# Optimization experiments

Measured on AMD Instinct MI355X. Metric: run time of the kernel, lower is better.

Reference implementation:

```python
import jax, jax.numpy as jnp
import numpy as np

B, T, D_MODEL = 2, 1024, 1024
HEAD_DIM = 128
NUM_HEADS = D_MODEL // HEAD_DIM          # 8
EXPAND_V = 1
HEAD_V = HEAD_DIM * EXPAND_V             # 128
KEY_DIM = NUM_HEADS * HEAD_DIM           # 1024
VALUE_DIM = NUM_HEADS * HEAD_V           # 1024
CONV_SIZE = 4
NUM_LEVELS = int(np.log2(T)) + 1         # 11 Fenwick levels
EPS = 1e-5
SCALE = HEAD_DIM ** -0.5


def setup_inputs() -> dict:
    ks = jax.random.split(jax.random.key(0), 20)
    w = lambda i, shp: 0.02 * jax.random.normal(ks[i], shp, jnp.float32)
    return {
        'x': jax.random.normal(ks[0], (B, T, D_MODEL), jnp.float32),
        'cos': jax.random.normal(ks[1], (T, HEAD_DIM), jnp.float32),
        'sin': jax.random.normal(ks[2], (T, HEAD_DIM), jnp.float32),
        'Wq': w(3, (D_MODEL, KEY_DIM)),
        'Wk': w(4, (D_MODEL, KEY_DIM)),
        'Wv': w(5, (D_MODEL, VALUE_DIM)),
        'Wb': w(6, (D_MODEL, NUM_HEADS)),
        'Wa': w(7, (D_MODEL, NUM_HEADS)),
        'Wl': w(8, (D_MODEL, NUM_HEADS * NUM_LEVELS)),
        'Wg': w(9, (D_MODEL, VALUE_DIM)),
        'Wo': w(10, (VALUE_DIM, D_MODEL)),
        'conv_q': 0.2 * jax.random.normal(ks[11], (KEY_DIM, CONV_SIZE), jnp.float32),
        'conv_k': 0.2 * jax.random.normal(ks[12], (KEY_DIM, CONV_SIZE), jnp.float32),
        'conv_v': 0.2 * jax.random.normal(ks[13], (VALUE_DIM, CONV_SIZE), jnp.float32),
        'A_log': jnp.log(jax.random.uniform(ks[14], (NUM_HEADS,), jnp.float32, 1.0, 16.0)),
        'dt_bias': jnp.log(jnp.expm1(jax.random.uniform(ks[15], (NUM_HEADS,), jnp.float32, 0.001, 0.1))),
        'norm_w': jnp.ones((HEAD_V,), jnp.float32),
    }


def _dwconv_silu(x, w):
    # causal depthwise conv1d (ShortConvolution, activation=silu). x:[B,T,C], w:[C,K]
    xp = jnp.pad(x, ((0, 0), (CONV_SIZE - 1, 0), (0, 0)))
    y = jax.lax.conv_general_dilated(xp, w.T[:, None, :], (1,), 'VALID',
                                     dimension_numbers=('NHC', 'HIO', 'NHC'),
                                     feature_group_count=w.shape[0])
    return jax.nn.silu(y)


def _l2norm(x):
    return x * jax.lax.rsqrt(jnp.sum(x * x, -1, keepdims=True) + 1e-6)


def _levels():
    # Fenwick-tree level of token s (0-indexed) in the prefix decomposition at time t:
    # level(t,s) = floor(log2((t+1) XOR s)) for s <= t.
    n = jnp.arange(1, T + 1, dtype=jnp.int32)[:, None]
    s = jnp.arange(T, dtype=jnp.int32)[None, :]
    xval = jnp.maximum(jnp.bitwise_xor(n, s), 1)
    lev = jnp.floor(jnp.log2(xval.astype(jnp.float32))).astype(jnp.int32)
    return jnp.clip(lev, 0, NUM_LEVELS - 1)  # [T,T]


def _forward(x, Wq, Wk, Wv, Wb, Wa, Wl, Wg, Wo, conv_q, conv_k, conv_v, A_log, dt_bias, norm_w):
    # projections + short conv + silu, split heads -> [B,H,T,d]
    q = _dwconv_silu(x @ Wq, conv_q).reshape(B, T, NUM_HEADS, HEAD_DIM).transpose(0, 2, 1, 3)
    k = _dwconv_silu(x @ Wk, conv_k).reshape(B, T, NUM_HEADS, HEAD_DIM).transpose(0, 2, 1, 3)
    v = _dwconv_silu(x @ Wv, conv_v).reshape(B, T, NUM_HEADS, HEAD_V).transpose(0, 2, 1, 3)
    q = _l2norm(q) * SCALE
    k = _l2norm(k)
    beta = jax.nn.sigmoid(x @ Wb).transpose(0, 2, 1)                      # [B,H,T]
    g = -jnp.exp(A_log) * jax.nn.softplus(x @ Wa + dt_bias)              # [B,T,H] log-decay per step
    gc = jnp.cumsum(g.transpose(0, 2, 1), axis=-1)                        # [B,H,T]
    lam = jax.nn.sigmoid(x @ Wl).reshape(B, T, NUM_HEADS, NUM_LEVELS).transpose(0, 2, 1, 3)  # [B,H,T,L]

    idx = jnp.arange(T)
    causal = idx[:, None] >= idx[None, :]
    strict = idx[:, None] > idx[None, :]
    # stable decay matrix D[t,s] = exp(gc_t - gc_s) <= 1 for s <= t
    logD = gc[..., :, None] - gc[..., None, :]
    Dm = jnp.exp(jnp.where(causal, logD, -jnp.inf))                       # [B,H,T,T]

    # WY / UT transform of the gated delta rule:
    #   u_t = beta_t * v_t - beta_t * sum_{s<t} (k_t . k_s) exp(gc_t-gc_s) u_s
    Akk = jnp.einsum('bhtd,bhsd->bhts', k, k) * Dm * strict
    u = jax.scipy.linalg.solve_triangular(beta[..., None] * Akk,
                                          beta[..., None] * v,
                                          lower=True, unit_diagonal=True)  # [B,H,T,dv]

    # log-linear (hierarchical) readout: o_t = sum_s lam_t[level(t,s)] * (q_t.k_s) D[t,s] * u_s
    P = jnp.einsum('bhtd,bhsd->bhts', q, k) * Dm
    M = jnp.take_along_axis(lam, _levels()[None, None], axis=3)           # [B,H,T,T]
    o = jnp.einsum('bhts,bhsd->bhtd', P * M, u).transpose(0, 2, 1, 3)      # [B,T,H,dv]

    # gated RMSNorm output gate, then output projection
    gate = (x @ Wg).reshape(B, T, NUM_HEADS, HEAD_V)
    o = o * jax.lax.rsqrt(jnp.mean(o * o, -1, keepdims=True) + EPS) * norm_w * jax.nn.silu(gate)
    return o.reshape(B, T, VALUE_DIM) @ Wo


def reference(x, cos, sin, Wq, Wk, Wv, Wb, Wa, Wl, Wg, Wo, conv_q, conv_k, conv_v, A_log, dt_bias, norm_w):
    # cos/sin are accepted (block signature) but unused, matching the source module.
    return _forward(x, Wq, Wk, Wv, Wb, Wa, Wl, Wg, Wo, conv_q, conv_k, conv_v, A_log, dt_bias, norm_w)
```

## Files before the change

### kernel.cpp

```cpp
#include <hip/hip_runtime.h>
#include <hip/hip_bf16.h>
#include <math.h>

#define SCALE_Q 0.08838834764831845f

typedef __bf16 bf16x8 __attribute__((ext_vector_type(8)));
typedef float f32x4 __attribute__((ext_vector_type(4)));

static __device__ __forceinline__ float sigm(float x){ return 1.f/(1.f+__expf(-x)); }
static __device__ __forceinline__ ushort f2b(float v){
  __hip_bfloat16 t = __float2bfloat16(v);
  return __builtin_bit_cast(ushort, t);
}

__global__ __launch_bounds__(256) void cast_x(const float* __restrict__ X,
    ushort* __restrict__ Y)
{
  int idx = blockIdx.x*256 + threadIdx.x;
  float4 v = *(const float4*)&X[(size_t)idx*4];
  ushort4 o; o.x=f2b(v.x); o.y=f2b(v.y); o.z=f2b(v.z); o.w=f2b(v.w);
  *(ushort4*)&Y[(size_t)idx*4] = o;
}

__global__ __launch_bounds__(256) void transcast(const float* __restrict__ W,
    ushort* __restrict__ Wt)
{
  __shared__ float tile[32][36];
  int n0 = blockIdx.x*32, k0 = blockIdx.y*32;
  int tid = threadIdx.x;
  int r = tid >> 3, c4 = (tid & 7) << 2;
  *(float4*)&tile[r][c4] = *(const float4*)&W[(size_t)(k0 + r)*1024 + n0 + c4];
  __syncthreads();
  ushort4 o;
  o.x = f2b(tile[c4+0][r]); o.y = f2b(tile[c4+1][r]);
  o.z = f2b(tile[c4+2][r]); o.w = f2b(tile[c4+3][r]);
  *(ushort4*)&Wt[(size_t)(n0 + r)*1024 + k0 + c4] = o;
}

__global__ __launch_bounds__(256) void copy_wsmall(const float* __restrict__ Wb,
    const float* __restrict__ Wa, const float* __restrict__ Wl, float* __restrict__ Wsm)
{
  int idx = blockIdx.x*256 + threadIdx.x;
  if (idx >= 1024*104) return;
  int k = idx / 104, c = idx % 104;
  float v = (c < 8) ? Wb[k*8+c] : (c < 16) ? Wa[k*8+(c-8)] : Wl[k*88+(c-16)];
  Wsm[idx] = v;
}

__global__ __launch_bounds__(256) void gemm_bf16(const ushort* __restrict__ A,
    const ushort* __restrict__ Bt, float* __restrict__ C0, float* __restrict__ C1,
    int M, int N, int K, int nsplit, int ld0, int ld1)
{
  __shared__ ushort As[128*32];
  __shared__ ushort Bs[128*32];
  int tid = threadIdx.x;
  int bm = blockIdx.y * 128, bn = blockIdx.x * 128;
  int wave = tid >> 6, lane = tid & 63;
  int wm = (wave >> 1) * 64, wn = (wave & 1) * 64;
  int l16 = lane & 15, kh = lane >> 4;
  f32x4 acc[4][4] = {};
  int rowA0 = tid >> 2, boA = (tid & 3) * 16;
  for (int k0 = 0; k0 < K; k0 += 32) {
    #pragma unroll
    for (int j = 0; j < 2; ++j) {
      int row = rowA0 + j*64;
      const char* gA = (const char*)A + (((size_t)(bm+row)*K + k0)*2 + boA);
      const char* gB = (const char*)Bt + (((size_t)(bn+row)*K + k0)*2 + boA);
      __builtin_amdgcn_global_load_lds((const __attribute__((address_space(1))) unsigned*)gA,
        (__attribute__((address_space(3))) unsigned*)((char*)As + row*64 + boA), 16, 0, 0);
      __builtin_amdgcn_global_load_lds((const __attribute__((address_space(1))) unsigned*)gB,
        (__attribute__((address_space(3))) unsigned*)((char*)Bs + row*64 + boA), 16, 0, 0);
    }
    __syncthreads();
    bf16x8 af[4], bfr[4];
    #pragma unroll
    for (int i = 0; i < 4; ++i)
      af[i] = *(bf16x8*)((char*)As + (wm + i*16 + l16)*64 + kh*16);
    #pragma unroll
    for (int j = 0; j < 4; ++j)
      bfr[j] = *(bf16x8*)((char*)Bs + (wn + j*16 + l16)*64 + kh*16);
    #pragma unroll
    for (int i = 0; i < 4; ++i)
      #pragma unroll
      for (int j = 0; j < 4; ++j)
        acc[i][j] = __builtin_amdgcn_mfma_f32_16x16x32_bf16(af[i], bfr[j], acc[i][j], 0, 0, 0);
    __syncthreads();
  }
  int rg = lane >> 4;
  #pragma unroll
  for (int i = 0; i < 4; ++i) {
    #pragma unroll
    for (int j = 0; j < 4; ++j) {
      int col = bn + wn + j*16 + l16;
      #pragma unroll
      for (int r = 0; r < 4; ++r) {
        int row = bm + wm + i*16 + rg*4 + r;
        float v = acc[i][j][r];
        if (col < nsplit) C0[(size_t)row*ld0 + col] = v;
        else              C1[(size_t)row*ld1 + (col - nsplit)] = v;
      }
    }
  }
}

__global__ __launch_bounds__(256) void skinny104(const float* __restrict__ X,
    const float* __restrict__ Wsm, float* __restrict__ part)
{
  __shared__ float XL[64][132];
  __shared__ float WsL[128][112];
  int tid = threadIdx.x;
  int m0 = blockIdx.x << 6;
  int k0 = blockIdx.y << 7;
  #pragma unroll
  for (int j = 0; j < 8; ++j) {
    int s = tid + j*256;
    int row = s >> 5, c4 = (s & 31) << 2;
    *(float4*)&XL[row][c4] = *(const float4*)&X[(size_t)(m0 + row)*1024 + k0 + c4];
  }
  {
    int k = tid >> 1, c = 104 + ((tid & 1) << 2);
    *(float4*)&WsL[k][c] = (float4){0.f,0.f,0.f,0.f};
  }
  {
    int k = tid >> 1, cb = (tid & 1) * 52;
    #pragma unroll
    for (int j = 0; j < 13; ++j) {
      *(float4*)&WsL[k][cb + j*4] = *(const float4*)&Wsm[(size_t)(k0 + k)*104 + cb + j*4];
    }
  }
  __syncthreads();
  int row = tid >> 2, cq = tid & 3;
  int cbase = cq * 28;
  f32x4 acc[7] = {};
  const float* xrow = &XL[row][0];
  #pragma unroll 4
  for (int k = 0; k < 128; ++k) {
    float xv = xrow[k];
    const f32x4* wr = (const f32x4*)&WsL[k][cbase];
    #pragma unroll
    for (int j = 0; j < 7; ++j) acc[j] += xv * wr[j];
  }
  float* pr = &part[((size_t)blockIdx.y*2048 + m0 + row)*104 + cbase];
  int nst = (cq == 3) ? 5 : 7;
  for (int j = 0; j < nst; ++j) *(f32x4*)&pr[j*4] = acc[j];
}

__global__ __launch_bounds__(256) void reduce8(const float* __restrict__ part,
    float* __restrict__ xs)
{
  int idx = blockIdx.x*256 + threadIdx.x;
  float s = 0.f;
  #pragma unroll
  for (int i = 0; i < 8; ++i) s += part[(size_t)i*212992 + idx];
  xs[idx] = s;
}

__global__ __launch_bounds__(256) void conv_silu(const float* __restrict__ X,
    const float* __restrict__ W, float* __restrict__ Yf, ushort* __restrict__ Yb,
    int mode, int ldx)
{
  int row = blockIdx.x;
  int b = row >> 10, t = row & 1023;
  int tid = threadIdx.x;
  int c0 = tid << 2;
  float w[4][4];
  #pragma unroll
  for (int c = 0; c < 4; ++c) {
    float4 wv = *(const float4*)&W[(c0 + c)*4];
    w[c][0]=wv.x; w[c][1]=wv.y; w[c][2]=wv.z; w[c][3]=wv.w;
  }
  float acc[4] = {0.f,0.f,0.f,0.f};
  #pragma unroll
  for (int j = 0; j < 4; ++j) {
    int tt = t - 3 + j;
    if (tt >= 0) {
      float4 xv = *(const float4*)&X[(size_t)(b*1024 + tt)*ldx + c0];
      acc[0] += w[0][j]*xv.x; acc[1] += w[1][j]*xv.y;
      acc[2] += w[2][j]*xv.z; acc[3] += w[3][j]*xv.w;
    }
  }
  #pragma unroll
  for (int c = 0; c < 4; ++c) acc[c] *= sigm(acc[c]);
  if (mode < 2) {
    float ss = acc[0]*acc[0]+acc[1]*acc[1]+acc[2]*acc[2]+acc[3]*acc[3];
    ss += __shfl_xor(ss, 1); ss += __shfl_xor(ss, 2); ss += __shfl_xor(ss, 4);
    ss += __shfl_xor(ss, 8); ss += __shfl_xor(ss, 16);
    float r = rsqrtf(ss + 1e-6f);
    if (mode == 0) r *= SCALE_Q;
    acc[0]*=r; acc[1]*=r; acc[2]*=r; acc[3]*=r;
  }
  size_t o = (size_t)(b*1024 + t)*1024 + c0;
  if (mode != 0) {
    float4 yv; yv.x=acc[0]; yv.y=acc[1]; yv.z=acc[2]; yv.w=acc[3];
    *(float4*)&Yf[o] = yv;
  }
  if (mode != 2) {
    ushort4 yb; yb.x=f2b(acc[0]); yb.y=f2b(acc[1]); yb.z=f2b(acc[2]); yb.w=f2b(acc[3]);
    *(ushort4*)&Yb[o] = yb;
  }
}

__global__ __launch_bounds__(256) void gc2(const float* __restrict__ xs,
    const float* __restrict__ A_log, const float* __restrict__ dt_bias,
    float* __restrict__ gc)
{
  int bh = blockIdx.x, b = bh >> 3, h = bh & 7;
  __shared__ float sc[256];
  int tid = threadIdx.x;
  float aexp = __expf(A_log[h]), db = dt_bias[h];
  int t0 = tid*4;
  float g[4], csum = 0.f;
  #pragma unroll
  for (int z = 0; z < 4; ++z) {
    float zv = xs[(size_t)(b*1024 + t0 + z)*104 + 8 + h] + db;
    float sp = (zv > 20.f) ? zv : log1pf(__expf(zv));
    csum += -aexp*sp;
    g[z] = csum;
  }
  sc[tid] = csum;
  __syncthreads();
  for (int ofs = 1; ofs < 256; ofs <<= 1) {
    float v = (tid >= ofs) ? sc[tid-ofs] : 0.f;
    __syncthreads();
    sc[tid] += v;
    __syncthreads();
  }
  float excl = sc[tid] - csum;
  #pragma unroll
  for (int z = 0; z < 4; ++z) gc[bh*1024 + t0 + z] = excl + g[z];
}

__global__ __launch_bounds__(256) void chunk_prep(const float* __restrict__ Kg,
    const float* __restrict__ Vg, const float* __restrict__ xs,
    const float* __restrict__ gcg, float* __restrict__ cw, ushort* __restrict__ cWk16,
    ushort* __restrict__ cKpT16, float* __restrict__ eD)
{
  int blk = blockIdx.x;
  int bh = blk >> 4, ck = blk & 15;
  int b = bh >> 3, h = bh & 7;
  int a = ck << 6;
  __shared__ float Kc[64][132];
  __shared__ float As[64][68];
  __shared__ float gcl[65];
  __shared__ float bl[64];
  __shared__ float egc[64];
  __shared__ float edt[64];
  int tid = threadIdx.x;
  for (int e = tid; e < 64*32; e += 256) {
    int t = e >> 5, c4 = (e & 31) << 2;
    *(float4*)&Kc[t][c4] = *(const float4*)&Kg[(size_t)(b*1024 + a + t)*1024 + h*128 + c4];
  }
  if (tid < 64) {
    gcl[tid] = gcg[bh*1024 + a + tid];
    bl[tid] = sigm(xs[(size_t)(b*1024 + a + tid)*104 + h]);
  }
  if (tid == 64) gcl[64] = (ck < 15) ? gcg[bh*1024 + a + 64] : 0.f;
  __syncthreads();
  if (tid < 64) {
    egc[tid] = __expf(gcl[tid] - gcl[0]);
    edt[tid] = (ck < 15) ? __expf(gcl[64] - gcl[tid]) : 0.f;
  }
  {
    int ti = tid >> 4, si = tid & 15;
    if (si <= ti) {
      float dot[4][4] = {};
      for (int kk = 0; kk < 128; kk += 4) {
        float4 kt[4], ks[4];
        #pragma unroll
        for (int z = 0; z < 4; ++z) kt[z] = *(float4*)&Kc[ti*4+z][kk];
        #pragma unroll
        for (int z = 0; z < 4; ++z) ks[z] = *(float4*)&Kc[si*4+z][kk];
        #pragma unroll
        for (int i = 0; i < 4; ++i)
          #pragma unroll
          for (int j = 0; j < 4; ++j)
            dot[i][j] += kt[i].x*ks[j].x + kt[i].y*ks[j].y + kt[i].z*ks[j].z + kt[i].w*ks[j].w;
      }
      #pragma unroll
      for (int i = 0; i < 4; ++i) {
        int t = ti*4 + i;
        #pragma unroll
        for (int j = 0; j < 4; ++j) {
          int s = si*4 + j;
          if (s < t) As[t][s] = bl[t]*dot[i][j]*__expf(gcl[t]-gcl[s]);
        }
      }
    }
  }
  __syncthreads();
  int c = tid;
  float u[64];
  if (c < 128) {
    #pragma unroll
    for (int t = 0; t < 64; ++t)
      u[t] = bl[t]*Vg[(size_t)(b*1024 + a + t)*1024 + h*128 + c];
  } else {
    int d = c - 128;
    #pragma unroll
    for (int t = 0; t < 64; ++t)
      u[t] = bl[t]*egc[t]*Kc[t][d];
  }
  #pragma unroll
  for (int t = 1; t < 64; ++t) {
    float acc = u[t];
    int s = 0;
    #pragma unroll
    for (; s + 4 <= t; s += 4) {
      float4 a4 = *(float4*)&As[t][s];
      acc -= a4.x*u[s] + a4.y*u[s+1] + a4.z*u[s+2] + a4.w*u[s+3];
    }
    #pragma unroll
    for (; s < t; ++s) acc -= As[t][s]*u[s];
    u[t] = acc;
  }
  size_t cbase = (size_t)blk*8192;
  if (c < 128) {
    #pragma unroll
    for (int t = 0; t < 64; ++t)
      cw[cbase + t*128 + c] = u[t];
  } else {
    int d = c - 128;
    #pragma unroll
    for (int t = 0; t < 64; ++t) {
      cWk16[cbase + t*128 + d] = f2b(-u[t]);
      cKpT16[cbase + d*64 + t] = f2b(Kc[t][d]*edt[t]);
    }
  }
  if (tid == 0) eD[blk] = (ck < 15) ? __expf(gcl[64]-gcl[0]) : 0.f;
}

__global__ __launch_bounds__(256) void chunk_scan6(const float* __restrict__ cw,
    const ushort* __restrict__ cWk16, const ushort* __restrict__ cKpT16,
    const float* __restrict__ eD, ushort* __restrict__ Ut)
{
  int blk = blockIdx.x;
  int slice = blk >> 4, bh = blk & 15;
  int e_base = slice << 3;
  __shared__ ushort Wks[2][8192];
  __shared__ ushort Kps[2][8192];
  __shared__ ushort StT[16*128];
  __shared__ ushort usT[16*64];
  __shared__ float  Stf[128*16];
  int tid = threadIdx.x;
  int wave = tid >> 6, lane = tid & 63;
  int l15 = lane & 15, kh = lane >> 4;
  for (int idx = tid; idx < 16*128; idx += 256) StT[idx] = 0;
  for (int idx = tid; idx < 16*64; idx += 256) usT[idx] = 0;
  for (int idx = tid; idx < 128*16; idx += 256) Stf[idx] = 0.f;

  int e = l15;
  int t0 = wave*16 + kh*4;
  int ci0 = bh << 4;
  f32x4 wcur = {0.f,0.f,0.f,0.f};
  if (e < 8) {
    #pragma unroll
    for (int r = 0; r < 4; ++r)
      wcur[r] = cw[(size_t)ci0*8192 + (t0+r)*128 + e_base + e];
  }
  {
    const char* wg = (const char*)(cWk16 + (size_t)ci0*8192);
    const char* kg = (const char*)(cKpT16 + (size_t)ci0*8192);
    #pragma unroll
    for (int j = 0; j < 4; ++j) {
      unsigned off = (j<<12) + (tid<<4);
      unsigned wrow = off >> 8, wslot = (off >> 4) & 15;
      unsigned wsrc = wrow*256 + ((wslot ^ (wrow & 15)) << 4);
      __builtin_amdgcn_global_load_lds((const __attribute__((address_space(1))) unsigned*)(wg + wsrc),
        (__attribute__((address_space(3))) unsigned*)((char*)&Wks[0][0] + off), 16, 0, 0);
      unsigned krow = off >> 7, kslot = (off >> 4) & 7;
      unsigned ksrc = krow*128 + ((kslot ^ (krow & 7)) << 4);
      __builtin_amdgcn_global_load_lds((const __attribute__((address_space(1))) unsigned*)(kg + ksrc),
        (__attribute__((address_space(3))) unsigned*)((char*)&Kps[0][0] + off), 16, 0, 0);
    }
  }
  __syncthreads();

  for (int i = 0; i < 16; ++i) {
    int ci = ci0 + i, a = i << 6, cur = i & 1;
    f32x4 wnext = {0.f,0.f,0.f,0.f};
    if (i < 15) {
      if (e < 8) {
        #pragma unroll
        for (int r = 0; r < 4; ++r)
          wnext[r] = cw[(size_t)(ci+1)*8192 + (t0+r)*128 + e_base + e];
      }
      const char* wg = (const char*)(cWk16 + (size_t)(ci+1)*8192);
      const char* kg = (const char*)(cKpT16 + (size_t)(ci+1)*8192);
      char* wl = (char*)&Wks[cur^1][0];
      char* kl = (char*)&Kps[cur^1][0];
      #pragma unroll
      for (int j = 0; j < 4; ++j) {
        unsigned off = (j<<12) + (tid<<4);
        unsigned wrow = off >> 8, wslot = (off >> 4) & 15;
        unsigned wsrc = wrow*256 + ((wslot ^ (wrow & 15)) << 4);
        __builtin_amdgcn_global_load_lds((const __attribute__((address_space(1))) unsigned*)(wg + wsrc),
          (__attribute__((address_space(3))) unsigned*)(wl + off), 16, 0, 0);
        unsigned krow = off >> 7, kslot = (off >> 4) & 7;
        unsigned ksrc = krow*128 + ((kslot ^ (krow & 7)) << 4);
        __builtin_amdgcn_global_load_lds((const __attribute__((address_space(1))) unsigned*)(kg + ksrc),
          (__attribute__((address_space(3))) unsigned*)(kl + off), 16, 0, 0);
      }
    }
    {
      f32x4 d = wcur;
      const char* wkb = (const char*)&Wks[cur][0];
      int arow = wave*16 + l15;
      #pragma unroll
      for (int ks = 0; ks < 4; ++ks) {
        bf16x8 afr = *(const bf16x8*)(wkb + arow*256 + (((ks*4 + kh) ^ l15) << 4));
        bf16x8 bfr = *(const bf16x8*)((const char*)StT + l15*256 + (((ks*4 + kh) ^ l15) << 4));
        d = __builtin_amdgcn_mfma_f32_16x16x32_bf16(afr, bfr, d, 0, 0, 0);
      }
      if (e < 8) {
        ushort4 uw;
        uw.x = f2b(d[0]); uw.y = f2b(d[1]); uw.z = f2b(d[2]); uw.w = f2b(d[3]);
        *(ushort4*)((char*)usT + e*128 + (((t0>>3) ^ (e&7)) << 4) + (t0&7)*2) = uw;
        *(ushort4*)&Ut[(size_t)(bh*128 + e_base + e)*1024 + a + t0] = uw;
      }
    }
    asm volatile("s_waitcnt lgkmcnt(0)" ::: "memory");
    __builtin_amdgcn_s_barrier();
    __builtin_amdgcn_sched_barrier(0);
    if (i < 15) {
      float ed = eD[ci];
      const char* kpb = (const char*)&Kps[cur][0];
      #pragma unroll
      for (int mt = 0; mt < 2; ++mt) {
        int krow = (wave*2 + mt)*16 + l15;
        int k0 = (wave*2 + mt)*16 + kh*4;
        f32x4 c;
        #pragma unroll
        for (int r = 0; r < 4; ++r) c[r] = ed * Stf[(k0+r)*16 + e];
        #pragma unroll
        for (int ts = 0; ts < 2; ++ts) {
          bf16x8 afr = *(const bf16x8*)(kpb + krow*128 + (((ts*4 + kh) ^ (krow&7)) << 4));
          bf16x8 bfr = *(const bf16x8*)((const char*)usT + l15*128 + (((ts*4 + kh) ^ (l15&7)) << 4));
          c = __builtin_amdgcn_mfma_f32_16x16x32_bf16(afr, bfr, c, 0, 0, 0);
        }
        #pragma unroll
        for (int r = 0; r < 4; ++r) Stf[(k0+r)*16 + e] = c[r];
        if (e < 8) {
          ushort4 sw;
          sw.x = f2b(c[0]); sw.y = f2b(c[1]); sw.z = f2b(c[2]); sw.w = f2b(c[3]);
          *(ushort4*)((char*)StT + e*256 + (((k0>>3) ^ e) << 4) + (k0&7)*2) = sw;
        }
      }
      wcur = wnext;
      asm volatile("s_waitcnt vmcnt(0) lgkmcnt(0)" ::: "memory");
      __builtin_amdgcn_s_barrier();
      __builtin_amdgcn_sched_barrier(0);
    }
  }
}

__global__ __launch_bounds__(256) void readout3(const ushort* __restrict__ Qb,
    const ushort* __restrict__ Kb, const ushort* __restrict__ Ut,
    const float* __restrict__ gcg, const float* __restrict__ xs,
    float* __restrict__ Og)
{
  int blk = blockIdx.x;
  int bh = blk >> 4, ic = blk & 15;
  int half = blockIdx.y;
  int b = bh >> 3, h = bh & 7;
  int tbase = ic << 6;
  __shared__ ushort Ks[2][8192];
  __shared__ ushort Us[2][8192];
  __shared__ ushort Pl[4][1024];
  __shared__ float lamS[64][12];
  int tid = threadIdx.x;
  int wave = tid >> 6, lane = tid & 63;
  int l15 = lane & 15, kh = lane >> 4;

  const char* kgb = (const char*)Kb + ((size_t)(b*1024)*1024 + h*128)*2;
  const char* ugb = (const char*)Ut + ((size_t)(bh*128)*1024)*2;

  for (int e = tid; e < 64*11; e += 256) {
    int t = e/11, l = e%11;
    lamS[t][l] = sigm(xs[(size_t)(b*1024+tbase+t)*104 + 16 + h*11 + l]);
  }
  int tl = kh*4;
  float gct_r[4];
  #pragma unroll
  for (int r = 0; r < 4; ++r) gct_r[r] = gcg[bh*1024 + tbase + wave*16 + tl + r];
  bf16x8 qf[4];
  {
    const ushort* qp = &Qb[(size_t)(b*1024 + tbase + wave*16 + l15)*1024 + h*128 + kh*8];
    #pragma unroll
    for (int kk = 0; kk < 4; ++kk) qf[kk] = *(const bf16x8*)(qp + kk*32);
  }

  f32x4 accO[8] = {};
  int nsteps = ic + 1;
  int jmid = (nsteps + 1) >> 1;
  int j0 = half ? jmid : 0;
  int j1 = half ? nsteps : jmid;
  ushort* Pw = &Pl[wave][0];

  if (j0 < j1) {
    {
      const char* kg = kgb + (size_t)(j0<<6)*2048;
      const char* ug = ugb + (size_t)(j0<<6)*2;
      #pragma unroll
      for (int it = 0; it < 4; ++it) {
        unsigned off = (it<<12) + (tid<<4);
        unsigned krow = off >> 8, kc = (off >> 4) & 15;
        unsigned ksrc = krow*2048 + ((kc ^ (krow & 15)) << 4);
        __builtin_amdgcn_global_load_lds((const __attribute__((address_space(1))) unsigned*)(kg + ksrc),
          (__attribute__((address_space(3))) unsigned*)((char*)&Ks[0][0] + off), 16, 0, 0);
        unsigned ud = off >> 7, uc = (off >> 4) & 7;
        unsigned usrc = ud*2048 + ((uc ^ (ud & 7)) << 4);
        __builtin_amdgcn_global_load_lds((const __attribute__((address_space(1))) unsigned*)(ug + usrc),
          (__attribute__((address_space(3))) unsigned*)((char*)&Us[0][0] + off), 16, 0, 0);
      }
    }
    __syncthreads();
    int cur = 0;
    for (int j = j0; j < j1; ++j) {
      int sbase = j << 6;
      if (j + 1 < j1) {
        const char* kg = kgb + (size_t)((j+1)<<6)*2048;
        const char* ug = ugb + (size_t)((j+1)<<6)*2;
        char* kl = (char*)&Ks[cur^1][0];
        char* ul = (char*)&Us[cur^1][0];
        #pragma unroll
        for (int it = 0; it < 4; ++it) {
          unsigned off = (it<<12) + (tid<<4);
          unsigned krow = off >> 8, kc = (off >> 4) & 15;
          unsigned ksrc = krow*2048 + ((kc ^ (krow & 15)) << 4);
          __builtin_amdgcn_global_load_lds((const __attribute__((address_space(1))) unsigned*)(kg + ksrc),
            (__attribute__((address_space(3))) unsigned*)(kl + off), 16, 0, 0);
          unsigned ud = off >> 7, uc = (off >> 4) & 7;
          unsigned usrc = ud*2048 + ((uc ^ (ud & 7)) << 4);
          __builtin_amdgcn_global_load_lds((const __attribute__((address_space(1))) unsigned*)(ug + usrc),
            (__attribute__((address_space(3))) unsigned*)(ul + off), 16, 0, 0);
        }
      }
      float gcs_r[4];
      #pragma unroll
      for (int jt = 0; jt < 4; ++jt)
        gcs_r[jt] = gcg[bh*1024 + sbase + jt*16 + l15];
      f32x4 accS[4] = {};
      const char* ksb = (const char*)&Ks[cur][0];
      #pragma unroll
      for (int jt = 0; jt < 4; ++jt) {
        int row = jt*16 + l15;
        int rsw = row & 15;
        #pragma unroll
        for (int kk = 0; kk < 4; ++kk) {
          bf16x8 kf = *(const bf16x8*)(ksb + row*256 + (((kk*4 + kh) ^ rsw) << 4));
          accS[jt] = __builtin_amdgcn_mfma_f32_16x16x32_bf16(qf[kk], kf, accS[jt], 0, 0, 0);
        }
      }
      #pragma unroll
      for (int jt = 0; jt < 4; ++jt) {
        int sg = sbase + jt*16 + l15;
        #pragma unroll
        for (int r = 0; r < 4; ++r) {
          int t_loc = tl + r;
          int tg = tbase + wave*16 + t_loc;
          float pv = 0.f;
          if (sg <= tg) {
            int lev = 31 - __clz((unsigned)((tg+1) ^ sg));
            lev = lev > 10 ? 10 : lev;
            pv = accS[jt][r] * __expf(gct_r[r] - gcs_r[jt]) * lamS[wave*16 + t_loc][lev];
          }
          int bo = (t_loc << 7) + ((jt*16 + l15) << 1);
          bo ^= (t_loc & 7) << 4;
          *(ushort*)((char*)Pw + bo) = f2b(pv);
        }
      }
      const char* usb = (const char*)&Us[cur][0];
      #pragma unroll
      for (int ks = 0; ks < 2; ++ks) {
        int bo = (l15 << 7) + ((ks*32 + kh*8) << 1);
        bo ^= (l15 & 7) << 4;
        bf16x8 pa = *(bf16x8*)((char*)Pw + bo);
        #pragma unroll
        for (int dt = 0; dt < 8; ++dt) {
          int d = dt*16 + l15;
          bf16x8 uf = *(const bf16x8*)(usb + d*128 + (((ks*4 + kh) ^ (d & 7)) << 4));
          accO[dt] = __builtin_amdgcn_mfma_f32_16x16x32_bf16(pa, uf, accO[dt], 0, 0, 0);
        }
      }
      __syncthreads();
      cur ^= 1;
    }
  }
  float* og = Og + (size_t)half*2097152;
  #pragma unroll
  for (int dt = 0; dt < 8; ++dt) {
    #pragma unroll
    for (int r = 0; r < 4; ++r) {
      int row = tbase + wave*16 + tl + r;
      og[(size_t)(b*1024 + row)*1024 + h*128 + dt*16 + l15] = accO[dt][r];
    }
  }
}

__global__ __launch_bounds__(64) void normgate(const float* __restrict__ O1,
    const float* __restrict__ O2, const float* __restrict__ G,
    const float* __restrict__ norm_w, ushort* __restrict__ Y)
{
  int row = blockIdx.x;
  int lane = threadIdx.x;
  size_t base = (size_t)(row >> 3)*1024 + (size_t)(row & 7)*128;
  float2 oa = *(const float2*)&O1[base + lane*2];
  float2 ob = *(const float2*)&O2[base + lane*2];
  float ox = oa.x + ob.x, oy = oa.y + ob.y;
  float ss = ox*ox + oy*oy;
  #pragma unroll
  for (int m = 1; m < 64; m <<= 1) ss += __shfl_xor(ss, m);
  float r = rsqrtf(ss * (1.f/128.f) + 1e-5f);
  float2 g = *(const float2*)&G[base + lane*2];
  ushort2 y;
  y.x = f2b(ox * r * norm_w[lane*2+0] * (g.x * sigm(g.x)));
  y.y = f2b(oy * r * norm_w[lane*2+1] * (g.y * sigm(g.y)));
  *(ushort2*)&Y[base + lane*2] = y;
}

extern "C" void kernel_launch(void* const* d_in, const int* in_sizes, int n_in,
                              void* d_out, int out_size, void* d_ws, size_t ws_size,
                              hipStream_t stream)
{
  const float* x    = (const float*)d_in[0];
  const float* Wq   = (const float*)d_in[3];
  const float* Wk   = (const float*)d_in[4];
  const float* Wv   = (const float*)d_in[5];
  const float* Wb   = (const float*)d_in[6];
  const float* Wa   = (const float*)d_in[7];
  const float* Wl   = (const float*)d_in[8];
  const float* Wg   = (const float*)d_in[9];
  const float* Wo   = (const float*)d_in[10];
  const float* cq   = (const float*)d_in[11];
  const float* ck   = (const float*)d_in[12];
  const float* cv   = (const float*)d_in[13];
  const float* A_log   = (const float*)d_in[14];
  const float* dt_bias = (const float*)d_in[15];
  const float* norm_w  = (const float*)d_in[16];
  float* out = (float*)d_out;

  float* p = (float*)d_ws;
  float* xqkv = p;  p += 6291456;
  float* xg   = p;  p += 2097152;
  float* kb   = p;  p += 2097152;
  float* vb   = p;  p += 2097152;
  float* o1   = p;  p += 2097152;
  float* o2   = p;  p += 2097152;
  float* xs   = p;  p += 212992;
  float* gc   = p;  p += 16384;
  float* eD   = p;  p += 256;
  ushort* x16 = (ushort*)p; p += 1048576;
  ushort* Wt4 = (ushort*)p; p += 2097152;
  ushort* Wot = (ushort*)p; p += 524288;
  float* Wsm  = p;  p += 106496;
  ushort* yb16= (ushort*)p; p += 1048576;
  ushort* qb16= (ushort*)p; p += 1048576;
  ushort* kb16= (ushort*)p; p += 1048576;
  ushort* ut16= (ushort*)p; p += 1048576;
  float* cw  = xqkv;
  ushort* cWk16  = (ushort*)(xqkv + 2097152);
  ushort* cKpT16 = (ushort*)(xqkv + 3145728);
  float* part = o1;

  dim3 blk(256);
  cast_x<<<dim3(2048), blk, 0, stream>>>(x, x16);
  transcast<<<dim3(32,32), blk, 0, stream>>>(Wq, Wt4);
  transcast<<<dim3(32,32), blk, 0, stream>>>(Wk, Wt4 + 1024*1024);
  transcast<<<dim3(32,32), blk, 0, stream>>>(Wv, Wt4 + 2*1024*1024);
  transcast<<<dim3(32,32), blk, 0, stream>>>(Wg, Wt4 + 3*1024*1024);
  transcast<<<dim3(32,32), blk, 0, stream>>>(Wo, Wot);
  copy_wsmall<<<dim3(416), blk, 0, stream>>>(Wb, Wa, Wl, Wsm);
  gemm_bf16<<<dim3(32,16), blk, 0, stream>>>(x16, Wt4, xqkv, xg, 2048, 4096, 1024,
                                             3072, 3072, 1024);
  skinny104<<<dim3(32,8), blk, 0, stream>>>(x, Wsm, part);
  reduce8<<<dim3(833), blk, 0, stream>>>(part, xs);
  conv_silu<<<dim3(2048), blk, 0, stream>>>(xqkv + 0,    cq, nullptr, qb16, 0, 3072);
  conv_silu<<<dim3(2048), blk, 0, stream>>>(xqkv + 1024, ck, kb, kb16, 1, 3072);
  conv_silu<<<dim3(2048), blk, 0, stream>>>(xqkv + 2048, cv, vb, nullptr, 2, 3072);
  gc2<<<dim3(16), blk, 0, stream>>>(xs, A_log, dt_bias, gc);
  chunk_prep<<<dim3(256), blk, 0, stream>>>(kb, vb, xs, gc, cw, cWk16, cKpT16, eD);
  chunk_scan6<<<dim3(256), blk, 0, stream>>>(cw, cWk16, cKpT16, eD, ut16);
  readout3<<<dim3(256,2), blk, 0, stream>>>(qb16, kb16, ut16, gc, xs, o1);
  normgate<<<dim3(16384), dim3(64), 0, stream>>>(o1, o2, xg, norm_w, yb16);
  gemm_bf16<<<dim3(8,16), blk, 0, stream>>>(yb16, Wot, out, out, 2048, 1024, 1024,
                                            1024, 1024, 1024);
}
```

Measured before the change: 210.7 us.

## Double-buffer GEMM LDS loads, swizzle workgroups, store QKV projection as bf16

The GEMM kernel now double-buffers its LDS tiles, issuing the next K-slice's global-to-LDS loads before computing on the current slice. This halves the barriers per iteration and overlaps load latency with MFMA work. It also remaps workgroup IDs in groups of eight to change cache locality across the grid. The QKV projection output is written as bf16 and the conv kernels read bf16, which cuts intermediate memory traffic at the cost of rounding pre-conv activations to bf16 precision.

After: 212.2 us. About the same (+0.7%).

```diff
diff --git a/kernel.cpp b/kernel.cpp
--- a/kernel.cpp
+++ b/kernel.cpp
@@ -11,6 +11,9 @@
 static __device__ __forceinline__ ushort f2b(float v){
   __hip_bfloat16 t = __float2bfloat16(v);
   return __builtin_bit_cast(ushort, t);
+}
+static __device__ __forceinline__ float b2f(ushort u){
+  unsigned v = (unsigned)u << 16; return __builtin_bit_cast(float, v);
 }
 
 __global__ __launch_bounds__(256) void cast_x(const float* __restrict__ X,
@@ -48,43 +51,68 @@
 }
 
 __global__ __launch_bounds__(256) void gemm_bf16(const ushort* __restrict__ A,
-    const ushort* __restrict__ Bt, float* __restrict__ C0, float* __restrict__ C1,
-    int M, int N, int K, int nsplit, int ld0, int ld1)
-{
-  __shared__ ushort As[128*32];
-  __shared__ ushort Bs[128*32];
+    const ushort* __restrict__ Bt, void* __restrict__ C0, float* __restrict__ C1,
+    int M, int N, int K, int nsplit, int ld0, int ld1, int c0bf16)
+{
+  __shared__ ushort As[2][128*32];
+  __shared__ ushort Bs[2][128*32];
   int tid = threadIdx.x;
-  int bm = blockIdx.y * 128, bn = blockIdx.x * 128;
+  int gx = gridDim.x;
+  int nwg = gx * gridDim.y;
+  int id = blockIdx.y * gx + blockIdx.x;
+  int id2 = (id & 7) * (nwg >> 3) + (id >> 3);
+  int bm = (id2 / gx) * 128, bn = (id2 % gx) * 128;
   int wave = tid >> 6, lane = tid & 63;
   int wm = (wave >> 1) * 64, wn = (wave & 1) * 64;
   int l16 = lane & 15, kh = lane >> 4;
   f32x4 acc[4][4] = {};
   int rowA0 = tid >> 2, boA = (tid & 3) * 16;
-  for (int k0 = 0; k0 < K; k0 += 32) {
+  int niter = K >> 5;
+
+  {
     #pragma unroll
     for (int j = 0; j < 2; ++j) {
       int row = rowA0 + j*64;
-      const char* gA = (const char*)A + (((size_t)(bm+row)*K + k0)*2 + boA);
-      const char* gB = (const char*)Bt + (((size_t)(bn+row)*K + k0)*2 + boA);
+      const char* gA = (const char*)A + (((size_t)(bm+row)*K)*2 + boA);
+      const char* gB = (const char*)Bt + (((size_t)(bn+row)*K)*2 + boA);
       __builtin_amdgcn_global_load_lds((const __attribute__((address_space(1))) unsigned*)gA,
-        (__attribute__((address_space(3))) unsigned*)((char*)As + row*64 + boA), 16, 0, 0);
+        (__attribute__((address_space(3))) unsigned*)((char*)&As[0][0] + row*64 + boA), 16, 0, 0);
       __builtin_amdgcn_global_load_lds((const __attribute__((address_space(1))) unsigned*)gB,
-        (__attribute__((address_space(3))) unsigned*)((char*)Bs + row*64 + boA), 16, 0, 0);
-    }
+        (__attribute__((address_space(3))) unsigned*)((char*)&Bs[0][0] + row*64 + boA), 16, 0, 0);
+    }
+  }
+  __syncthreads();
+  int cur = 0;
+  for (int i = 0; i < niter; ++i) {
+    if (i + 1 < niter) {
+      int k0 = (i+1) << 5;
+      char* al = (char*)&As[cur^1][0];
+      char* bl = (char*)&Bs[cur^1][0];
+      #pragma unroll
+      for (int j = 0; j < 2; ++j) {
+        int row = rowA0 + j*64;
+        const char* gA = (const char*)A + (((size_t)(bm+row)*K + k0)*2 + boA);
+        const char* gB = (const char*)Bt + (((size_t)(bn+row)*K + k0)*2 + boA);
+        __builtin_amdgcn_global_load_lds((const __attribute__((address_space(1))) unsigned*)gA,
+          (__attribute__((address_space(3))) unsigned*)(al + row*64 + boA), 16, 0, 0);
+        __builtin_amdgcn_global_load_lds((const __attribute__((address_space(1))) unsigned*)gB,
+          (__attribute__((address_space(3))) unsigned*)(bl + row*64 + boA), 16, 0, 0);
+      }
+    }
+    bf16x8 af[4], bfr[4];
+    #pragma unroll
+    for (int ii = 0; ii < 4; ++ii)
+      af[ii] = *(bf16x8*)((char*)&As[cur][0] + (wm + ii*16 + l16)*64 + kh*16);
+    #pragma unroll
+    for (int j = 0; j < 4; ++j)
+      bfr[j] = *(bf16x8*)((char*)&Bs[cur][0] + (wn + j*16 + l16)*64 + kh*16);
+    #pragma unroll
+    for (int ii = 0; ii < 4; ++ii)
+      #pragma unroll
+      for (int j = 0; j < 4; ++j)
+        acc[ii][j] = __builtin_amdgcn_mfma_f32_16x16x32_bf16(af[ii], bfr[j], acc[ii][j], 0, 0, 0);
     __syncthreads();
-    bf16x8 af[4], bfr[4];
-    #pragma unroll
-    for (int i = 0; i < 4; ++i)
-      af[i] = *(bf16x8*)((char*)As + (wm + i*16 + l16)*64 + kh*16);
-    #pragma unroll
-    for (int j = 0; j < 4; ++j)
-      bfr[j] = *(bf16x8*)((char*)Bs + (wn + j*16 + l16)*64 + kh*16);
-    #pragma unroll
-    for (int i = 0; i < 4; ++i)
-      #pragma unroll
-      for (int j = 0; j < 4; ++j)
-        acc[i][j] = __builtin_amdgcn_mfma_f32_16x16x32_bf16(af[i], bfr[j], acc[i][j], 0, 0, 0);
-    __syncthreads();
+    cur ^= 1;
   }
   int rg = lane >> 4;
   #pragma unroll
@@ -96,8 +124,10 @@
       for (int r = 0; r < 4; ++r) {
         int row = bm + wm + i*16 + rg*4 + r;
         float v = acc[i][j][r];
-        if (col < nsplit) C0[(size_t)row*ld0 + col] = v;
-        else              C1[(size_t)row*ld1 + (col - nsplit)] = v;
+        if (col < nsplit) {
+          if (c0bf16) ((ushort*)C0)[(size_t)row*ld0 + col] = f2b(v);
+          else        ((float*)C0)[(size_t)row*ld0 + col] = v;
+        } else C1[(size_t)row*ld1 + (col - nsplit)] = v;
       }
     }
   }
@@ -155,7 +185,7 @@
   xs[idx] = s;
 }
 
-__global__ __launch_bounds__(256) void conv_silu(const float* __restrict__ X,
+__global__ __launch_bounds__(256) void conv_silu(const ushort* __restrict__ X,
     const float* __restrict__ W, float* __restrict__ Yf, ushort* __restrict__ Yb,
     int mode, int ldx)
 {
@@ -174,9 +204,9 @@
   for (int j = 0; j < 4; ++j) {
     int tt = t - 3 + j;
     if (tt >= 0) {
-      float4 xv = *(const float4*)&X[(size_t)(b*1024 + tt)*ldx + c0];
-      acc[0] += w[0][j]*xv.x; acc[1] += w[1][j]*xv.y;
-      acc[2] += w[2][j]*xv.z; acc[3] += w[3][j]*xv.w;
+      ushort4 xv = *(const ushort4*)&X[(size_t)(b*1024 + tt)*ldx + c0];
+      acc[0] += w[0][j]*b2f(xv.x); acc[1] += w[1][j]*b2f(xv.y);
+      acc[2] += w[2][j]*b2f(xv.z); acc[3] += w[3][j]*b2f(xv.w);
     }
   }
   #pragma unroll
@@ -657,6 +687,7 @@
   ushort* qb16= (ushort*)p; p += 1048576;
   ushort* kb16= (ushort*)p; p += 1048576;
   ushort* ut16= (ushort*)p; p += 1048576;
+  ushort* xqkv16 = (ushort*)xqkv;
   float* cw  = xqkv;
   ushort* cWk16  = (ushort*)(xqkv + 2097152);
   ushort* cKpT16 = (ushort*)(xqkv + 3145728);
@@ -670,18 +701,18 @@
   transcast<<<dim3(32,32), blk, 0, stream>>>(Wg, Wt4 + 3*1024*1024);
   transcast<<<dim3(32,32), blk, 0, stream>>>(Wo, Wot);
   copy_wsmall<<<dim3(416), blk, 0, stream>>>(Wb, Wa, Wl, Wsm);
-  gemm_bf16<<<dim3(32,16), blk, 0, stream>>>(x16, Wt4, xqkv, xg, 2048, 4096, 1024,
-                                             3072, 3072, 1024);
+  gemm_bf16<<<dim3(32,16), blk, 0, stream>>>(x16, Wt4, xqkv16, xg, 2048, 4096, 1024,
+                                             3072, 3072, 1024, 1);
   skinny104<<<dim3(32,8), blk, 0, stream>>>(x, Wsm, part);
   reduce8<<<dim3(833), blk, 0, stream>>>(part, xs);
-  conv_silu<<<dim3(2048), blk, 0, stream>>>(xqkv + 0,    cq, nullptr, qb16, 0, 3072);
-  conv_silu<<<dim3(2048), blk, 0, stream>>>(xqkv + 1024, ck, kb, kb16, 1, 3072);
-  conv_silu<<<dim3(2048), blk, 0, stream>>>(xqkv + 2048, cv, vb, nullptr, 2, 3072);
+  conv_silu<<<dim3(2048), blk, 0, stream>>>(xqkv16 + 0,    cq, nullptr, qb16, 0, 3072);
+  conv_silu<<<dim3(2048), blk, 0, stream>>>(xqkv16 + 1024, ck, kb, kb16, 1, 3072);
+  conv_silu<<<dim3(2048), blk, 0, stream>>>(xqkv16 + 2048, cv, vb, nullptr, 2, 3072);
   gc2<<<dim3(16), blk, 0, stream>>>(xs, A_log, dt_bias, gc);
   chunk_prep<<<dim3(256), blk, 0, stream>>>(kb, vb, xs, gc, cw, cWk16, cKpT16, eD);
   chunk_scan6<<<dim3(256), blk, 0, stream>>>(cw, cWk16, cKpT16, eD, ut16);
   readout3<<<dim3(256,2), blk, 0, stream>>>(qb16, kb16, ut16, gc, xs, o1);
   normgate<<<dim3(16384), dim3(64), 0, stream>>>(o1, o2, xg, norm_w, yb16);
   gemm_bf16<<<dim3(8,16), blk, 0, stream>>>(yb16, Wot, out, out, 2048, 1024, 1024,
-                                            1024, 1024, 1024);
-}
+                                            1024, 1024, 1024, 0);
+}
```
